# Kernel optimization log

Hardware: AMD Instinct MI355X
Metric: run time of the kernel (lower is better)

The kernel has to match this reference:

```python
import jax, jax.numpy as jnp
import numpy as np

NUM_ELMT = 64
INPUT_DIM = 16
BOUND = 50.0
MESH_RATIO = 1.2
N_POINTS = 1_048_576


def _build_mesh():
    m = NUM_ELMT
    one_step = BOUND * (MESH_RATIO - 1.0) / (MESH_RATIO ** (m / 2) - 1.0)
    idx = np.arange(-m / 2, m / 2 + 1)
    mesh = (MESH_RATIO ** np.abs(idx) - 1.0) / (MESH_RATIO - 1.0) * one_step * np.sign(idx)
    mesh_norm = (mesh + BOUND) / (2.0 * BOUND)
    mesh_norm = np.concatenate([[0.0], mesh_norm[1:-1], [1.0]]).astype(np.float32)
    elmt_size = (mesh_norm[1:] - mesh_norm[:-1]).astype(np.float32)
    return jnp.asarray(mesh_norm), jnp.asarray(elmt_size)


def setup_inputs() -> dict:
    key = jax.random.key(0)
    k1, k2 = jax.random.split(key)
    x = jax.random.uniform(k1, (N_POINTS, INPUT_DIM), jnp.float32, minval=-BOUND, maxval=BOUND)
    pdj = jnp.ones((N_POINTS, 1), jnp.float32)
    sldj = jnp.zeros((N_POINTS, 1), jnp.float32)
    log_p = 0.1 * jax.random.normal(k2, (NUM_ELMT - 1, INPUT_DIM), jnp.float32)
    mesh_norm, elmt_size = _build_mesh()
    return {"x": x, "pdj": pdj, "sldj": sldj, "log_p": log_p,
            "mesh_norm": mesh_norm, "elmt_size": elmt_size}


def _normalize_pdf(log_p, elmt_size):
    # elmt_size: (M,) -> (M,1) column, log_p: (M-1, D)
    es = elmt_size[:, None]
    ep = jnp.exp(log_p)
    px = ep * (es[:-1] + es[1:]) / 2.0
    px = ep * (1.0 - es[0]) / jnp.sum(px, axis=0, keepdims=True)
    p0 = jnp.ones((1, log_p.shape[1]), log_p.dtype)
    pdf_norm = jnp.concatenate([p0, px, p0], axis=0)            # (M+1, D)
    cell = (pdf_norm[:-1] + pdf_norm[1:]) / 2.0 * es            # (M, D)
    # F_ref[i] = sum(cell[:i]); single cumsum instead of the O(M^2) torch loop
    F_ref = jnp.concatenate([jnp.zeros_like(p0), jnp.cumsum(cell, axis=0)[:-1]], axis=0)  # (M, D)
    return pdf_norm, F_ref


def reference(x, pdj, sldj, log_p, mesh_norm, elmt_size):
    pdf_norm, F_ref = _normalize_pdf(log_p, elmt_size)
    xn = (x + BOUND) / (2.0 * BOUND)                            # (N, D) in [0,1]
    k = jnp.searchsorted(mesh_norm, xn, side='left')            # (N, D), torch right=False
    cover = (k != 0) & (k != NUM_ELMT + 1)
    k = jnp.clip(k, 1, NUM_ELMT)
    km1 = k - 1
    v1 = jnp.take_along_axis(pdf_norm, km1, axis=0)             # pdf at lower node
    v2 = jnp.take_along_axis(pdf_norm, k, axis=0)               # pdf at upper node
    xmodi = xn - mesh_norm[km1]                                 # offset inside element
    h = elmt_size[km1]                                          # element width
    F_pre = jnp.take_along_axis(F_ref, km1, axis=0)             # CDF at lower node
    y = jnp.where(cover, F_pre + xmodi * xmodi * 0.5 * (v2 - v1) / h + xmodi * v1, xn)
    abs_det = jnp.where(cover, xmodi * (v2 - v1) / h + v1, 1.0)
    pdj_out = pdj * jnp.prod(abs_det, axis=-1, keepdims=True)
    sldj_out = sldj + jnp.sum(jnp.log(abs_det), axis=-1, keepdims=True)
    x_out = y * 2.0 * BOUND - BOUND
    return (x_out, pdj_out, sldj_out)
```

## Files before the change

### kernel.cpp

```cpp
#include <hip/hip_runtime.h>
#include <math.h>
#include <stdint.h>


namespace {
constexpr int DIM = 16;
constexpr int ME  = 64;
constexpr float BOUNDF = 50.0f;
constexpr float K1      = 6.8164378f;
constexpr float INV_L2R = 3.8017840f;
constexpr int NBIN = 66;
constexpr int ROWF = 68;
constexpr int COEF_FLOATS = NBIN * ROWF;
constexpr int BLOCK = 512;
}

__global__ __launch_bounds__(BLOCK) void nll_kernel(
    const float* __restrict__ x,
    const float* __restrict__ pdj,
    const float* __restrict__ sldj,
    const float* __restrict__ log_p,
    const float* __restrict__ mesh_norm,
    float* __restrict__ out,
    int npts, int npairs)
{
  __shared__ __align__(16) float co[COEF_FLOATS];

  const int tid  = threadIdx.x;
  const int wv   = tid >> 6;
  const int lane = tid & 63;

  const int t = blockIdx.x * BLOCK + tid;
  const bool live = t < npairs;

  const float4* __restrict__ x4 = reinterpret_cast<const float4*>(x);
  float4 xa, xb;
  float ps = 0.f;
  if (live) {
    xa = x4[2 * t];
    xb = x4[2 * t + 1];
    ps = (t & 1) ? sldj[t >> 1] : pdj[t >> 1];
  }

  {
    const float mj  = mesh_norm[lane];
    const float mj1 = mesh_norm[lane + 1];
    const float mj2 = mesh_norm[(lane + 2 > ME) ? ME : (lane + 2)];
    const float es0 = mesh_norm[1];
    const float h = mj1 - mj;
#pragma unroll
    for (int i = 0; i < 2; ++i) {
      const int d = 2 * wv + i;
      const float ep = (lane < 63) ? __expf(log_p[lane * DIM + d]) : 0.f;
      float ss = (lane < 63) ? ep * (mj2 - mj) : 0.f;
      ss += __shfl_xor(ss, 1);  ss += __shfl_xor(ss, 2);  ss += __shfl_xor(ss, 4);
      ss += __shfl_xor(ss, 8);  ss += __shfl_xor(ss, 16); ss += __shfl_xor(ss, 32);
      const float scale = (1.0f - es0) / (0.5f * ss);
      const float cur = (lane < 63) ? ep * scale : 1.0f;
      float prev = __shfl_up(cur, 1);
      if (lane == 0) prev = 1.0f;
      const float cell = (prev + cur) * 0.5f * h;
      float v = cell, o;
      o = __shfl_up(v, 1);  if (lane >= 1)  v += o;
      o = __shfl_up(v, 2);  if (lane >= 2)  v += o;
      o = __shfl_up(v, 4);  if (lane >= 4)  v += o;
      o = __shfl_up(v, 8);  if (lane >= 8)  v += o;
      o = __shfl_up(v, 16); if (lane >= 16) v += o;
      o = __shfl_up(v, 32); if (lane >= 32) v += o;
      const float F = v - cell;
      const float A = 0.5f * (cur - prev) / h;
      const float B = fmaf(-(A + A), mj, prev);
      const float D = fmaf(mj, fmaf(mj, A, -prev), F);
      *reinterpret_cast<float4*>(&co[(lane + 1) * ROWF + 4 * d]) =
          make_float4(A, B, D, A + A);
    }
    if (tid < 32) {
      const int row = (tid >> 4) ? (NBIN - 1) : 0;
      const int d = tid & 15;
      *reinterpret_cast<float4*>(&co[row * ROWF + 4 * d]) =
          make_float4(0.f, 1.f, 0.f, 0.f);
    }
  }
  __syncthreads();

  if (!live) return;

  float4* __restrict__ out4 = reinterpret_cast<float4*>(out);
  const int np16 = npts * DIM;
  const int p  = t >> 1;
  const int hh = t & 1;
  const int dbase = hh << 5;
  const float vals[8] = {xa.x, xa.y, xa.z, xa.w, xb.x, xb.y, xb.z, xb.w};

  float xn[8];
  int   idx[8];
#pragma unroll
  for (int j = 0; j < 8; ++j) {
    const float val = vals[j];
    xn[j] = fmaf(val, 0.01f, 0.5f);
    const float u = fmaf(fabsf(val), K1, 1.0f);
    const float n = __log2f(u) * INV_L2R;
    int k = 32 + (int)ceilf(copysignf(n, val));
    k = k < 0 ? 0 : (k > NBIN - 1 ? NBIN - 1 : k);
    idx[j] = k * ROWF + dbase + (j << 2);
  }

  float4 cf[8];
#pragma unroll
  for (int j = 0; j < 8; ++j)
    cf[j] = *reinterpret_cast<const float4*>(&co[idx[j]]);

  float yv[8], dt[8];
#pragma unroll
  for (int j = 0; j < 8; ++j) {
    const float z = xn[j];
    yv[j] = fmaf(fmaf(z, fmaf(z, cf[j].x, cf[j].y), cf[j].z), 2.0f * BOUNDF, -BOUNDF);
    dt[j] = fmaf(z, cf[j].w, cf[j].y);
  }
  const float prod = ((dt[0] * dt[1]) * (dt[2] * dt[3])) *
                     ((dt[4] * dt[5]) * (dt[6] * dt[7]));

  out4[2 * t]     = make_float4(yv[0], yv[1], yv[2], yv[3]);
  out4[2 * t + 1] = make_float4(yv[4], yv[5], yv[6], yv[7]);

  const float full = prod * __shfl_xor(prod, 1);
  const float res  = hh ? (ps + __logf(full)) : (ps * full);
  out[np16 + hh * npts + p] = res;
}

extern "C" void kernel_launch(void* const* d_in, const int* in_sizes, int n_in,
                              void* d_out, int out_size, void* d_ws, size_t ws_size,
                              hipStream_t stream) {
  const float* x    = (const float*)d_in[0];
  const float* pdj  = (const float*)d_in[1];
  const float* sldj = (const float*)d_in[2];
  const float* lp   = (const float*)d_in[3];
  const float* mesh = (const float*)d_in[4];
  float* out = (float*)d_out;

  const int npts   = in_sizes[0] / DIM;
  const int npairs = npts * 2;
  const int grid   = (npairs + BLOCK - 1) / BLOCK;

  hipLaunchKernelGGL(nll_kernel, dim3(grid), dim3(BLOCK), 0, stream,
                     x, pdj, sldj, lp, mesh, out, npts, npairs);
}
```

Baseline: 32.53 us.

## Persistent grid with double-buffered global-to-LDS staging of x and pdj/sldj

Caps the grid at 1024 blocks of 256 threads and turns the kernel into a persistent grid-stride loop. Each wave prefetches its next 64-pair tile of x and pdj/sldj straight into LDS with global_load_lds, using double buffering and manual vmcnt waits, while it computes the current tile. The per-block coefficient table is built once per block and reused over many tiles instead of once per 512 points. The cost is more LDS use, reliance on the hardware vmcnt ordering through hand-written waits, and extra shuffles to combine per-point products across four lanes.

Measured after the change: 39.74 us. 22.2% more time.

```diff
diff --git a/kernel.cpp b/kernel.cpp
--- a/kernel.cpp
+++ b/kernel.cpp
@@ -12,7 +12,21 @@
 constexpr int NBIN = 66;
 constexpr int ROWF = 68;
 constexpr int COEF_FLOATS = NBIN * ROWF;
-constexpr int BLOCK = 512;
+constexpr int BLOCK = 256;
+constexpr int NWAVE = 4;
+constexpr int STAGF = 576;
+constexpr int GRID_CAP = 1024;
+}
+
+__device__ __forceinline__ void gl_lds16(const float* g, float* l) {
+  __builtin_amdgcn_global_load_lds(
+      (const __attribute__((address_space(1))) void*)g,
+      (__attribute__((address_space(3))) void*)l, 16, 0, 0);
+}
+__device__ __forceinline__ void gl_lds4(const float* g, float* l) {
+  __builtin_amdgcn_global_load_lds(
+      (const __attribute__((address_space(1))) void*)g,
+      (__attribute__((address_space(3))) void*)l, 4, 0, 0);
 }
 
 __global__ __launch_bounds__(BLOCK) void nll_kernel(
@@ -25,22 +39,31 @@
     int npts, int npairs)
 {
   __shared__ __align__(16) float co[COEF_FLOATS];
+  __shared__ __align__(16) float stag[NWAVE * 2 * STAGF];
 
   const int tid  = threadIdx.x;
   const int wv   = tid >> 6;
   const int lane = tid & 63;
+  const int tpg  = gridDim.x * BLOCK;
 
-  const int t = blockIdx.x * BLOCK + tid;
-  const bool live = t < npairs;
+  float* stg[2] = {&stag[(wv * 2 + 0) * STAGF], &stag[(wv * 2 + 1) * STAGF]};
 
-  const float4* __restrict__ x4 = reinterpret_cast<const float4*>(x);
-  float4 xa, xb;
-  float ps = 0.f;
-  if (live) {
-    xa = x4[2 * t];
-    xb = x4[2 * t + 1];
-    ps = (t & 1) ? sldj[t >> 1] : pdj[t >> 1];
-  }
+  auto stage_issue = [&](int T, float* buf) {
+    int gi = 8 * T + 4 * lane;
+    const int gmax = 8 * npairs - 4;
+    int g0 = gi <= gmax ? gi : gmax;
+    int g1 = (gi + 256) <= gmax ? gi + 256 : gmax;
+    gl_lds16(x + g0, buf);
+    gl_lds16(x + g1, buf + 256);
+    const int P = T >> 1;
+    int pi = P + (lane & 31); if (pi >= npts) pi = npts - 1;
+    gl_lds4((lane < 32 ? pdj : sldj) + pi, buf + 512);
+  };
+
+  int T = blockIdx.x * BLOCK + wv * 64;
+  const bool wave_live = T < npairs;
+  if (wave_live) stage_issue(T, stg[0]);
+  __builtin_amdgcn_sched_barrier(0);
 
   {
     const float mj  = mesh_norm[lane];
@@ -49,8 +72,8 @@
     const float es0 = mesh_norm[1];
     const float h = mj1 - mj;
 #pragma unroll
-    for (int i = 0; i < 2; ++i) {
-      const int d = 2 * wv + i;
+    for (int i = 0; i < 4; ++i) {
+      const int d = 4 * wv + i;
       const float ep = (lane < 63) ? __expf(log_p[lane * DIM + d]) : 0.f;
       float ss = (lane < 63) ? ep * (mj2 - mj) : 0.f;
       ss += __shfl_xor(ss, 1);  ss += __shfl_xor(ss, 2);  ss += __shfl_xor(ss, 4);
@@ -83,49 +106,68 @@
   }
   __syncthreads();
 
-  if (!live) return;
+  if (!wave_live) return;
 
   float4* __restrict__ out4 = reinterpret_cast<float4*>(out);
   const int np16 = npts * DIM;
-  const int p  = t >> 1;
-  const int hh = t & 1;
-  const int dbase = hh << 5;
-  const float vals[8] = {xa.x, xa.y, xa.z, xa.w, xb.x, xb.y, xb.z, xb.w};
 
-  float xn[8];
-  int   idx[8];
+  auto do_group = [&](int g, const float* sbuf, int Tb) {
+    const int half = lane >> 1;
+    const int q    = lane & 1;
+    const int tt   = Tb + g * 32 + half;
+    const bool vld = tt < npairs;
+    const float4 xv = *reinterpret_cast<const float4*>(&sbuf[g * 256 + 4 * lane]);
+    const int hh = half & 1;
+    const int dbase = hh * 32 + q * 16;
+    const float vals[4] = {xv.x, xv.y, xv.z, xv.w};
+    float xn[4]; int idx[4];
 #pragma unroll
-  for (int j = 0; j < 8; ++j) {
-    const float val = vals[j];
-    xn[j] = fmaf(val, 0.01f, 0.5f);
-    const float u = fmaf(fabsf(val), K1, 1.0f);
-    const float n = __log2f(u) * INV_L2R;
-    int k = 32 + (int)ceilf(copysignf(n, val));
-    k = k < 0 ? 0 : (k > NBIN - 1 ? NBIN - 1 : k);
-    idx[j] = k * ROWF + dbase + (j << 2);
+    for (int j = 0; j < 4; ++j) {
+      const float val = vals[j];
+      xn[j] = fmaf(val, 0.01f, 0.5f);
+      const float u = fmaf(fabsf(val), K1, 1.0f);
+      const float n = __log2f(u) * INV_L2R;
+      int k = 32 + (int)ceilf(copysignf(n, val));
+      k = k < 0 ? 0 : (k > NBIN - 1 ? NBIN - 1 : k);
+      idx[j] = k * ROWF + dbase + (j << 2);
+    }
+    float4 cf[4];
+#pragma unroll
+    for (int j = 0; j < 4; ++j)
+      cf[j] = *reinterpret_cast<const float4*>(&co[idx[j]]);
+    float yv[4], dt[4];
+#pragma unroll
+    for (int j = 0; j < 4; ++j) {
+      const float z = xn[j];
+      yv[j] = fmaf(fmaf(z, fmaf(z, cf[j].x, cf[j].y), cf[j].z), 2.0f * BOUNDF, -BOUNDF);
+      dt[j] = fmaf(z, cf[j].w, cf[j].y);
+    }
+    float pr = (dt[0] * dt[1]) * (dt[2] * dt[3]);
+    if (vld) out4[2 * Tb + g * 64 + lane] = make_float4(yv[0], yv[1], yv[2], yv[3]);
+    pr *= __shfl_xor(pr, 1);
+    pr *= __shfl_xor(pr, 2);
+    const int pw = g * 16 + (lane >> 2);
+    const int p  = (Tb >> 1) + pw;
+    if (vld && (lane & 3) == 0) out[np16 + p] = sbuf[512 + pw] * pr;
+    if (vld && (lane & 3) == 1) out[np16 + npts + p] = sbuf[544 + pw] + __logf(pr);
+  };
+
+  int b = 0;
+  while (T < npairs) {
+    const int Tn = T + tpg;
+    if (Tn < npairs) {
+      stage_issue(Tn, stg[b ^ 1]);
+      __builtin_amdgcn_sched_barrier(0);
+      asm volatile("s_waitcnt vmcnt(3)" ::: "memory");
+    } else {
+      asm volatile("s_waitcnt vmcnt(0)" ::: "memory");
+    }
+    __builtin_amdgcn_sched_barrier(0);
+    do_group(0, stg[b], T);
+    do_group(1, stg[b], T);
+    T = Tn; b ^= 1;
   }
-
-  float4 cf[8];
-#pragma unroll
-  for (int j = 0; j < 8; ++j)
-    cf[j] = *reinterpret_cast<const float4*>(&co[idx[j]]);
-
-  float yv[8], dt[8];
-#pragma unroll
-  for (int j = 0; j < 8; ++j) {
-    const float z = xn[j];
-    yv[j] = fmaf(fmaf(z, fmaf(z, cf[j].x, cf[j].y), cf[j].z), 2.0f * BOUNDF, -BOUNDF);
-    dt[j] = fmaf(z, cf[j].w, cf[j].y);
-  }
-  const float prod = ((dt[0] * dt[1]) * (dt[2] * dt[3])) *
-                     ((dt[4] * dt[5]) * (dt[6] * dt[7]));
-
-  out4[2 * t]     = make_float4(yv[0], yv[1], yv[2], yv[3]);
-  out4[2 * t + 1] = make_float4(yv[4], yv[5], yv[6], yv[7]);
-
-  const float full = prod * __shfl_xor(prod, 1);
-  const float res  = hh ? (ps + __logf(full)) : (ps * full);
-  out[np16 + hh * npts + p] = res;
+  asm volatile("s_waitcnt vmcnt(0)" ::: "memory");
 }
 
 extern "C" void kernel_launch(void* const* d_in, const int* in_sizes, int n_in,
@@ -140,7 +182,8 @@
 
   const int npts   = in_sizes[0] / DIM;
   const int npairs = npts * 2;
-  const int grid   = (npairs + BLOCK - 1) / BLOCK;
+  int grid = (npairs + BLOCK - 1) / BLOCK;
+  if (grid > GRID_CAP) grid = GRID_CAP;
 
   hipLaunchKernelGGL(nll_kernel, dim3(grid), dim3(BLOCK), 0, stream,
                      x, pdj, sldj, lp, mesh, out, npts, npairs);
```

## Process one full point per thread instead of splitting across a thread pair

Applied to the files above, without the earlier changes.

Each thread now loads all 16 dimensions of a point (four float4 loads) and computes the full product and log itself, with no shuffle between paired threads. This halves the grid size, so the per-block shared-memory coefficient table is rebuilt in half as many blocks. In exchange each thread needs more registers, thread-level parallelism drops, and each thread's float4 accesses now span 64 contiguous bytes, which can make memory access less coalesced.

New measurement: 39.40 us. 21.1% more time.

```diff
diff --git a/kernel.cpp b/kernel.cpp
--- a/kernel.cpp
+++ b/kernel.cpp
@@ -22,7 +22,7 @@
     const float* __restrict__ log_p,
     const float* __restrict__ mesh_norm,
     float* __restrict__ out,
-    int npts, int npairs)
+    int npts)
 {
   __shared__ __align__(16) float co[COEF_FLOATS];
 
@@ -30,16 +30,19 @@
   const int wv   = tid >> 6;
   const int lane = tid & 63;
 
-  const int t = blockIdx.x * BLOCK + tid;
-  const bool live = t < npairs;
+  const int p = blockIdx.x * BLOCK + tid;
+  const bool live = p < npts;
 
   const float4* __restrict__ x4 = reinterpret_cast<const float4*>(x);
-  float4 xa, xb;
-  float ps = 0.f;
+  float4 X0, X1, X2, X3;
+  float pv = 0.f, sv = 0.f;
   if (live) {
-    xa = x4[2 * t];
-    xb = x4[2 * t + 1];
-    ps = (t & 1) ? sldj[t >> 1] : pdj[t >> 1];
+    X0 = x4[4 * p + 0];
+    X1 = x4[4 * p + 1];
+    X2 = x4[4 * p + 2];
+    X3 = x4[4 * p + 3];
+    pv = pdj[p];
+    sv = sldj[p];
   }
 
   {
@@ -87,45 +90,49 @@
 
   float4* __restrict__ out4 = reinterpret_cast<float4*>(out);
   const int np16 = npts * DIM;
-  const int p  = t >> 1;
-  const int hh = t & 1;
-  const int dbase = hh << 5;
-  const float vals[8] = {xa.x, xa.y, xa.z, xa.w, xb.x, xb.y, xb.z, xb.w};
 
-  float xn[8];
-  int   idx[8];
+  float vals[16];
+  *reinterpret_cast<float4*>(&vals[0])  = X0;
+  *reinterpret_cast<float4*>(&vals[4])  = X1;
+  *reinterpret_cast<float4*>(&vals[8])  = X2;
+  *reinterpret_cast<float4*>(&vals[12]) = X3;
+
+  float xn[16];
+  int   idx[16];
 #pragma unroll
-  for (int j = 0; j < 8; ++j) {
+  for (int j = 0; j < 16; ++j) {
     const float val = vals[j];
     xn[j] = fmaf(val, 0.01f, 0.5f);
     const float u = fmaf(fabsf(val), K1, 1.0f);
     const float n = __log2f(u) * INV_L2R;
     int k = 32 + (int)ceilf(copysignf(n, val));
     k = k < 0 ? 0 : (k > NBIN - 1 ? NBIN - 1 : k);
-    idx[j] = k * ROWF + dbase + (j << 2);
+    idx[j] = k * ROWF + (j << 2);
   }
 
-  float4 cf[8];
+  float4 cf[16];
 #pragma unroll
-  for (int j = 0; j < 8; ++j)
+  for (int j = 0; j < 16; ++j)
     cf[j] = *reinterpret_cast<const float4*>(&co[idx[j]]);
 
-  float yv[8], dt[8];
+  float yv[16], dt[16];
 #pragma unroll
-  for (int j = 0; j < 8; ++j) {
+  for (int j = 0; j < 16; ++j) {
     const float z = xn[j];
     yv[j] = fmaf(fmaf(z, fmaf(z, cf[j].x, cf[j].y), cf[j].z), 2.0f * BOUNDF, -BOUNDF);
     dt[j] = fmaf(z, cf[j].w, cf[j].y);
   }
-  const float prod = ((dt[0] * dt[1]) * (dt[2] * dt[3])) *
-                     ((dt[4] * dt[5]) * (dt[6] * dt[7]));
+  const float prod = (((dt[0] * dt[1]) * (dt[2] * dt[3])) *
+                      ((dt[4] * dt[5]) * (dt[6] * dt[7]))) *
+                     (((dt[8] * dt[9]) * (dt[10] * dt[11])) *
+                      ((dt[12] * dt[13]) * (dt[14] * dt[15])));
 
-  out4[2 * t]     = make_float4(yv[0], yv[1], yv[2], yv[3]);
-  out4[2 * t + 1] = make_float4(yv[4], yv[5], yv[6], yv[7]);
-
-  const float full = prod * __shfl_xor(prod, 1);
-  const float res  = hh ? (ps + __logf(full)) : (ps * full);
-  out[np16 + hh * npts + p] = res;
+  out4[4 * p + 0] = make_float4(yv[0],  yv[1],  yv[2],  yv[3]);
+  out4[4 * p + 1] = make_float4(yv[4],  yv[5],  yv[6],  yv[7]);
+  out4[4 * p + 2] = make_float4(yv[8],  yv[9],  yv[10], yv[11]);
+  out4[4 * p + 3] = make_float4(yv[12], yv[13], yv[14], yv[15]);
+  out[np16 + p]        = pv * prod;
+  out[np16 + npts + p] = sv + __logf(prod);
 }
 
 extern "C" void kernel_launch(void* const* d_in, const int* in_sizes, int n_in,
@@ -138,10 +145,9 @@
   const float* mesh = (const float*)d_in[4];
   float* out = (float*)d_out;
 
-  const int npts   = in_sizes[0] / DIM;
-  const int npairs = npts * 2;
-  const int grid   = (npairs + BLOCK - 1) / BLOCK;
+  const int npts = in_sizes[0] / DIM;
+  const int grid = (npts + BLOCK - 1) / BLOCK;
 
   hipLaunchKernelGGL(nll_kernel, dim3(grid), dim3(BLOCK), 0, stream,
-                     x, pdj, sldj, lp, mesh, out, npts, npairs);
+                     x, pdj, sldj, lp, mesh, out, npts);
 }
```
